# Optimization experiments

Hardware: AMD Instinct MI355X
Metric: run time of the kernel (lower is better)

Reference implementation:

```python
import jax, jax.numpy as jnp
import numpy as np
import math

B, TQ, TK, D = 4, 1024, 1024, 1024
H, DK, DV = 16, 64, 64


def _ln(x, g, b, eps=1e-5):
    m = x.mean(-1, keepdims=True)
    v = ((x - m) ** 2).mean(-1, keepdims=True)
    return (x - m) * jax.lax.rsqrt(v + eps) * g + b


def setup_inputs() -> dict:
    key = jax.random.key(0)
    ks = jax.random.split(key, 24)
    s = 0.02
    inp = {
        "x": jax.random.normal(ks[0], (B, TQ, D), jnp.float32),
        "y": jax.random.normal(ks[1], (B, TK, D), jnp.float32),
        "mask": jax.random.randint(ks[2], (B, TK), 0, 2).astype(bool),
        # pre-attention layernorms (affine)
        "ln1_g": jnp.ones((D,)), "ln1_b": jnp.zeros((D,)),
        "ln2_g": jnp.ones((D,)), "ln2_b": jnp.zeros((D,)),
        # mha1 projections
        "q_w": jax.random.normal(ks[3], (D, H * DK)) * s, "q_b": jnp.zeros((H * DK,)),
        "k_w": jax.random.normal(ks[4], (D, H * DK)) * s, "k_b": jnp.zeros((H * DK,)),
        "v_w": jax.random.normal(ks[5], (D, H * DV)) * s, "v_b": jnp.zeros((H * DV,)),
        "o_w": jax.random.normal(ks[6], (H * DV, D)) * s, "o_b": jnp.zeros((D,)),
        # MLP: [LN, ReLU, Linear] x 2 over sizes [D, D, D]
        "mln1_g": jnp.ones((D,)), "mln1_b": jnp.zeros((D,)),
        "l1_w": jax.random.normal(ks[7], (D, D)) * s, "l1_b": jnp.zeros((D,)),
        "mln2_g": jnp.ones((D,)), "mln2_b": jnp.zeros((D,)),
        "l2_w": jax.random.normal(ks[8], (D, D)) * s, "l2_b": jnp.zeros((D,)),
    }
    return inp


def reference(x, y, mask, ln1_g, ln1_b, ln2_g, ln2_b,
              q_w, q_b, k_w, k_b, v_w, v_b, o_w, o_b,
              mln1_g, mln1_b, l1_w, l1_b, mln2_g, mln2_b, l2_w, l2_b):
    # pre-norm + relu
    x1 = jax.nn.relu(_ln(x, ln1_g, ln1_b))
    y1 = jax.nn.relu(_ln(y, ln2_g, ln2_b))
    # cross attention (mha1)
    b, t, _ = x1.shape
    q = (x1 @ q_w + q_b).reshape(b, t, H, DK)
    k = (y1 @ k_w + k_b).reshape(b, -1, H, DK)
    v = (y1 @ v_w + v_b).reshape(b, -1, H, DV)
    logits = jnp.einsum('bthd,bThd->bhtT', q, k) * (1.0 / math.sqrt(DK))
    logits = jnp.where(mask[:, None, None, :], logits, -1e30)
    w = jax.nn.softmax(logits, axis=-1)
    attn = jnp.einsum('bhtT,bThd->bthd', w, v).reshape(b, t, H * DV)
    x = x + (attn @ o_w + o_b)
    # MLP: LN -> ReLU -> Linear, twice
    h = jax.nn.relu(_ln(x, mln1_g, mln1_b)) @ l1_w + l1_b
    out = jax.nn.relu(_ln(h, mln2_g, mln2_b)) @ l2_w + l2_b
    return out
```

## Files before the change

kernel.cpp:

```cpp
#include <hip/hip_runtime.h>
#include <hip/hip_bf16.h>
#include <math.h>

#define D_MODEL 1024
#define NTOK    4096

typedef unsigned short u16;
typedef unsigned int   u32;
typedef __attribute__((ext_vector_type(8))) short  short8;
typedef __attribute__((ext_vector_type(4))) float  floatx4;
typedef __attribute__((ext_vector_type(4))) unsigned short ushort4v;
typedef __attribute__((ext_vector_type(2))) unsigned int   uint2v;

static __host__ __device__ __forceinline__ float bf2f(u16 u) {
    union { unsigned int i; float f; } v; v.i = ((unsigned int)u) << 16; return v.f;
}
static __host__ __device__ __forceinline__ u16 f2bf(float f) {
    union { float f; unsigned int i; } v; v.f = f;
    unsigned int r = (v.i + 0x7FFFu + ((v.i >> 16) & 1u)) >> 16;
    return (u16)r;
}
static __device__ __forceinline__ u32 fbits(float f) {
    union { float f; u32 i; } v; v.f = f; return v.i;
}
static __device__ __forceinline__ void gl2lds16(const void* g, void* l) {
    __builtin_amdgcn_global_load_lds(
        (const __attribute__((address_space(1))) void*)g,
        (__attribute__((address_space(3))) void*)l, 16, 0, 0);
}

__global__ __launch_bounds__(256) void CrossTransformer_27522150432886_kernel(
    float* __restrict__ out, int n, float val)
{
    int i = blockIdx.x * 256 + threadIdx.x;
    if (i < n) out[i] = val;
}

__global__ __launch_bounds__(256) void mask_k(
    const void* __restrict__ mp, float* __restrict__ madd)
{
    const unsigned int* w = (const unsigned int*)mp;
    const int t = threadIdx.x;
    int bad = 0;
    for (int i = t; i < 1024; i += 256) {
        unsigned int v = w[i];
        if (!(v == 0u || v == 1u || v == 0xFFu || v == 0xFFFFFFFFu)) bad++;
    }
#pragma unroll
    for (int off = 32; off > 0; off >>= 1) bad += __shfl_xor(bad, off, 64);
    __shared__ int rb[4];
    if ((t & 63) == 0) rb[t >> 6] = bad;
    __syncthreads();
    const int Bc = rb[0] + rb[1] + rb[2] + rb[3];
    if (Bc * 2 > 1024) {
        const unsigned char* b8 = (const unsigned char*)mp;
        for (int i = t; i < 4096; i += 256) madd[i] = b8[i] ? 0.f : -1e30f;
    } else {
        const int* m32 = (const int*)mp;
        for (int i = t; i < 4096; i += 256) madd[i] = m32[i] ? 0.f : -1e30f;
    }
}

__global__ __launch_bounds__(256) void ln_relu_k(
    const void* __restrict__ in, const float* __restrict__ gam,
    const float* __restrict__ bet, u16* __restrict__ out, int bf16in)
{
    const int row = blockIdx.x, t = threadIdx.x;
    float v0, v1, v2, v3;
    if (bf16in) {
        ushort4v u = *(const ushort4v*)((const u16*)in + (size_t)row * D_MODEL + t * 4);
        v0 = bf2f(u[0]); v1 = bf2f(u[1]); v2 = bf2f(u[2]); v3 = bf2f(u[3]);
    } else {
        const float4 p = *(const float4*)((const float*)in + (size_t)row * D_MODEL + t * 4);
        v0 = p.x; v1 = p.y; v2 = p.z; v3 = p.w;
    }
    float s = v0 + v1 + v2 + v3;
    float q = v0 * v0 + v1 * v1 + v2 * v2 + v3 * v3;
#pragma unroll
    for (int off = 32; off > 0; off >>= 1) {
        s += __shfl_xor(s, off, 64);
        q += __shfl_xor(q, off, 64);
    }
    __shared__ float red[2][4];
    if ((t & 63) == 0) { red[0][t >> 6] = s; red[1][t >> 6] = q; }
    __syncthreads();
    s = red[0][0] + red[0][1] + red[0][2] + red[0][3];
    q = red[1][0] + red[1][1] + red[1][2] + red[1][3];

    const float mean = s * (1.0f / D_MODEL);
    const float var  = q * (1.0f / D_MODEL) - mean * mean;
    const float rstd = rsqrtf(var + 1e-5f);

    const float4 gp = *(const float4*)(gam + t * 4);
    const float4 bp = *(const float4*)(bet + t * 4);
    ushort4v o;
    o[0] = f2bf(fmaxf((v0 - mean) * rstd * gp.x + bp.x, 0.f));
    o[1] = f2bf(fmaxf((v1 - mean) * rstd * gp.y + bp.y, 0.f));
    o[2] = f2bf(fmaxf((v2 - mean) * rstd * gp.z + bp.z, 0.f));
    o[3] = f2bf(fmaxf((v3 - mean) * rstd * gp.w + bp.w, 0.f));
    *(ushort4v*)(out + (size_t)row * D_MODEL + t * 4) = o;
}

struct W6 { const float* w[6]; };
__global__ __launch_bounds__(256) void wtrans_k(W6 wp, u16* __restrict__ WtBase)
{
    __shared__ u16 tile[32][33];
    const float* W  = wp.w[blockIdx.z];
    u16*         Wt = WtBase + (size_t)blockIdx.z * D_MODEL * D_MODEL;
    const int c0 = blockIdx.x * 32, r0 = blockIdx.y * 32;
    const int tx = threadIdx.x, ty = threadIdx.y;
#pragma unroll
    for (int j = 0; j < 4; j++)
        tile[ty + j * 8][tx] = f2bf(W[(size_t)(r0 + ty + j * 8) * D_MODEL + c0 + tx]);
    __syncthreads();
#pragma unroll
    for (int j = 0; j < 4; j++)
        Wt[(size_t)(c0 + ty + j * 8) * D_MODEL + r0 + tx] = tile[tx][ty + j * 8];
}

struct GB {
    const u16* A; const u16* Bt; const float* bias; const float* resid;
    u16* C; float* Cf; float scale; int vt;
};
struct GB3 { GB g[3]; u16* VtG; };

__global__ __launch_bounds__(256) void gemm_qkv_k(GB3 gb)
{
    const GB cfg = gb.g[blockIdx.z];
    __shared__ __align__(16) u16 sm[3 * 8192];
    const int t = threadIdx.x, lane = t & 63, w = t >> 6;
    const int wy = w >> 1, wx = w & 1;
    const int bm = blockIdx.y * 128, bn = blockIdx.x * 128;
    const int m = lane & 15, g = lane >> 4;
    const int arow = t >> 2, aseg = (t & 3) * 8;

    const u16* Ag = cfg.A  + (size_t)(bm + arow) * D_MODEL + aseg;
    const u16* Bg = cfg.Bt + (size_t)(bn + arow) * D_MODEL + aseg;

    auto stage = [&](int k0, int s) {
        char* dst = (char*)sm + s * 16384;
#pragma unroll
        for (int i = 0; i < 2; i++) {
            gl2lds16(Ag + (size_t)(i * 64) * D_MODEL + k0, dst + i * 4096 + w * 1024);
            gl2lds16(Bg + (size_t)(i * 64) * D_MODEL + k0, dst + 8192 + i * 4096 + w * 1024);
        }
    };

    floatx4 acc[4][4] = {};
    const int NT = D_MODEL / 32;

    stage(0, 0);
    stage(32, 1);
    asm volatile("s_waitcnt vmcnt(4)" ::: "memory");
    __builtin_amdgcn_s_barrier();

    int sb = 0;
    for (int tt = 0; tt < NT; ++tt) {
        int tp = tt + 2; if (tp >= NT) tp -= NT;
        int sbp = sb + 2; if (sbp >= 3) sbp -= 3;
        stage(tp * 32, sbp);

        const u16* As = sm + sb * 8192;
        const u16* Bs = As + 4096;
        short8 af[4], bf[4];
#pragma unroll
        for (int mt = 0; mt < 4; mt++)
            af[mt] = *(const short8*)(As + (wy * 64 + mt * 16 + m) * 32 + g * 8);
#pragma unroll
        for (int nt = 0; nt < 4; nt++)
            bf[nt] = *(const short8*)(Bs + (wx * 64 + nt * 16 + m) * 32 + g * 8);

        __builtin_amdgcn_s_setprio(1);
#pragma unroll
        for (int mt = 0; mt < 4; mt++)
#pragma unroll
            for (int nt = 0; nt < 4; nt++)
                acc[mt][nt] = __builtin_amdgcn_mfma_f32_16x16x32_bf16(
                    af[mt], bf[nt], acc[mt][nt], 0, 0, 0);
        __builtin_amdgcn_s_setprio(0);

        asm volatile("s_waitcnt vmcnt(4)" ::: "memory");
        __builtin_amdgcn_s_barrier();
        sb = sb + 1; if (sb >= 3) sb -= 3;
    }
    asm volatile("s_waitcnt vmcnt(0)" ::: "memory");
    __builtin_amdgcn_s_barrier();

    float bv[4];
#pragma unroll
    for (int nt = 0; nt < 4; nt++)
        bv[nt] = cfg.bias[bn + wx * 64 + nt * 16 + m];

    if (!cfg.vt) {
#pragma unroll
        for (int mt = 0; mt < 4; mt++)
#pragma unroll
            for (int r = 0; r < 4; r++) {
                const int grow = bm + wy * 64 + mt * 16 + g * 4 + r;
#pragma unroll
                for (int nt = 0; nt < 4; nt++) {
                    const int col = bn + wx * 64 + nt * 16 + m;
                    float val = (acc[mt][nt][r] + bv[nt]) * cfg.scale;
                    cfg.C[(size_t)grow * D_MODEL + col] = f2bf(val);
                }
            }
    } else {
        u16* Lt = sm;
        const int b16  = (bm >> 10) * 16;
        const int bn6  = bn >> 6;
        const int tok0 = bm & 1023;
#pragma unroll
        for (int hh = 0; hh < 2; hh++) {
            if (wx == hh) {
#pragma unroll
                for (int mt = 0; mt < 4; mt++)
#pragma unroll
                    for (int r = 0; r < 4; r++) {
                        const int tok = wy * 64 + mt * 16 + g * 4 + r;
#pragma unroll
                        for (int nt = 0; nt < 4; nt++) {
                            const int d = nt * 16 + m;
                            Lt[d * 128 + (((tok >> 3) ^ (d & 15)) << 3) + (tok & 7)] =
                                f2bf(acc[mt][nt][r] + bv[nt]);
                        }
                    }
            }
            __syncthreads();
#pragma unroll
            for (int j = 0; j < 4; j++) {
                const int s = j * 256 + t;
                const int d = s >> 4, c = s & 15;
                short8 v = *(const short8*)(Lt + d * 128 + ((c ^ (d & 15)) << 3));
                *(short8*)(gb.VtG + ((size_t)((b16 + bn6 + hh) * 64 + d)) * 1024 + tok0 + c * 8) = v;
            }
            __syncthreads();
        }
    }
}

__global__ __launch_bounds__(256) void gemm_k(GB3 gb)
{
    const GB cfg = gb.g[blockIdx.z];
    __shared__ __align__(16) u16 sm[3 * 6144];
    const int t = threadIdx.x, lane = t & 63, w = t >> 6;
    const int wy = w >> 1, wx = w & 1;
    const int bm = blockIdx.y * 128, bn = blockIdx.x * 64;
    const int m = lane & 15, g = lane >> 4;

    const u16* Ag = cfg.A  + (size_t)(bm + (t >> 2)) * D_MODEL + (t & 3) * 8;
    const u16* Bg = cfg.Bt + (size_t)(bn + w * 16 + (lane >> 2)) * D_MODEL + (lane & 3) * 8;

    auto stage = [&](int k0, int s) {
        char* dst = (char*)sm + s * 12288;
#pragma unroll
        for (int i = 0; i < 2; i++)
            gl2lds16(Ag + (size_t)(i * 64) * D_MODEL + k0, dst + i * 4096 + w * 1024);
        gl2lds16(Bg + k0, dst + 8192 + w * 1024);
    };

    floatx4 acc[4][2] = {};
    const int NT = D_MODEL / 32;

    stage(0, 0);
    stage(32, 1);
    asm volatile("s_waitcnt vmcnt(3)" ::: "memory");
    __builtin_amdgcn_s_barrier();

    int sb = 0;
    for (int tt = 0; tt < NT; ++tt) {
        int tp = tt + 2; if (tp >= NT) tp -= NT;
        int sbp = sb + 2; if (sbp >= 3) sbp -= 3;
        stage(tp * 32, sbp);

        const u16* As = sm + sb * 6144;
        const u16* Bs = As + 4096;
        short8 af[4], bf[2];
#pragma unroll
        for (int mt = 0; mt < 4; mt++)
            af[mt] = *(const short8*)(As + (wy * 64 + mt * 16 + m) * 32 + g * 8);
#pragma unroll
        for (int nt = 0; nt < 2; nt++)
            bf[nt] = *(const short8*)(Bs + (wx * 32 + nt * 16 + m) * 32 + g * 8);

        __builtin_amdgcn_s_setprio(1);
#pragma unroll
        for (int mt = 0; mt < 4; mt++)
#pragma unroll
            for (int nt = 0; nt < 2; nt++)
                acc[mt][nt] = __builtin_amdgcn_mfma_f32_16x16x32_bf16(
                    af[mt], bf[nt], acc[mt][nt], 0, 0, 0);
        __builtin_amdgcn_s_setprio(0);

        asm volatile("s_waitcnt vmcnt(3)" ::: "memory");
        __builtin_amdgcn_s_barrier();
        sb = sb + 1; if (sb >= 3) sb -= 3;
    }
    asm volatile("s_waitcnt vmcnt(0)" ::: "memory");

    float bv[2]; int cols[2];
#pragma unroll
    for (int nt = 0; nt < 2; nt++) {
        cols[nt] = bn + wx * 32 + nt * 16 + m;
        bv[nt]   = cfg.bias[cols[nt]];
    }
#pragma unroll
    for (int mt = 0; mt < 4; mt++) {
#pragma unroll
        for (int r = 0; r < 4; r++) {
            const int grow = bm + wy * 64 + mt * 16 + g * 4 + r;
#pragma unroll
            for (int nt = 0; nt < 2; nt++) {
                float val = (acc[mt][nt][r] + bv[nt]) * cfg.scale;
                if (cfg.resid) val += cfg.resid[(size_t)grow * D_MODEL + cols[nt]];
                if (cfg.Cf) cfg.Cf[(size_t)grow * D_MODEL + cols[nt]] = val;
                else        cfg.C [(size_t)grow * D_MODEL + cols[nt]] = f2bf(val);
            }
        }
    }
}

__global__ __launch_bounds__(256) void attn_k(
    const u16* __restrict__ Q, const u16* __restrict__ Kk,
    const u16* __restrict__ VtG, const float* __restrict__ maddG,
    u16* __restrict__ Ob)
{
    __shared__ __align__(16) char smraw[41472];
    u16*   Ks   = (u16*)smraw;
    u16*   Vt   = (u16*)(smraw + 9216);
    u16*   Ps   = (u16*)(smraw + 18432);
    float* madd = (float*)(smraw + 36864);
    float* liS  = (float*)(smraw + 40960);

    const int qt = blockIdx.x, h = blockIdx.y, b = blockIdx.z;
    const int t = threadIdx.x, lane = t & 63, w = t >> 6;
    const int m = lane & 15, g = lane >> 4;

    for (int i = t; i < 1024; i += 256) madd[i] = maddG[b * 1024 + i];

    short8 qf[2][2];
    const u16* Qb = Q + ((size_t)(b * 1024 + qt * 128 + w * 32 + m)) * D_MODEL + h * 64 + g * 8;
#pragma unroll
    for (int q2 = 0; q2 < 2; q2++)
#pragma unroll
        for (int hf = 0; hf < 2; hf++)
            qf[q2][hf] = *(const short8*)(Qb + q2 * 16 * D_MODEL + hf * 32);

    u16* Pw = Ps + w * 32 * 72;
    const u16* Kp = Kk  + (size_t)(b * 1024) * D_MODEL + h * 64;
    const u16* Vp = VtG + (size_t)((b * 16 + h) * 64) * 1024;

    floatx4 Ov[2][4] = {};
    float li[2] = { 0.f, 0.f };

    for (int kt = 0; kt < 1024; kt += 64) {
#pragma unroll
        for (int i = 0; i < 2; i++) {
            const int s = i * 256 + t, row = s >> 3, seg = (s & 7) * 8;
            *(short8*)(Ks + row * 72 + seg) =
                *(const short8*)(Kp + (size_t)(kt + row) * D_MODEL + seg);
            *(short8*)(Vt + row * 72 + seg) =
                *(const short8*)(Vp + (size_t)row * 1024 + kt + seg);
        }
        __syncthreads();

        short8 af[4][2];
        float4 md[4];
#pragma unroll
        for (int tile = 0; tile < 4; tile++) {
            af[tile][0] = *(const short8*)(Ks + (tile * 16 + m) * 72 + g * 8);
            af[tile][1] = *(const short8*)(Ks + (tile * 16 + m) * 72 + 32 + g * 8);
            md[tile]    = *(const float4*)(madd + kt + tile * 16 + g * 4);
        }

#pragma unroll
        for (int q2 = 0; q2 < 2; q2++) {
            floatx4 st[4];
#pragma unroll
            for (int tile = 0; tile < 4; tile++) {
                floatx4 z = {};
                z = __builtin_amdgcn_mfma_f32_16x16x32_bf16(af[tile][0], qf[q2][0], z, 0, 0, 0);
                st[tile] = __builtin_amdgcn_mfma_f32_16x16x32_bf16(af[tile][1], qf[q2][1], z, 0, 0, 0);
            }
            float rs = 0.f;
#pragma unroll
            for (int tile = 0; tile < 4; tile++) {
                float p0 = exp2f(st[tile][0] + md[tile].x);
                float p1 = exp2f(st[tile][1] + md[tile].y);
                float p2 = exp2f(st[tile][2] + md[tile].z);
                float p3 = exp2f(st[tile][3] + md[tile].w);
                rs += (p0 + p1) + (p2 + p3);
                uint2v pk;
                pk[0] = __builtin_amdgcn_perm(fbits(p1), fbits(p0), 0x07060302u);
                pk[1] = __builtin_amdgcn_perm(fbits(p3), fbits(p2), 0x07060302u);
                *(uint2v*)(Pw + (q2 * 16 + m) * 72 + tile * 16 + g * 4) = pk;
            }
            rs += __shfl_xor(rs, 16, 64);
            rs += __shfl_xor(rs, 32, 64);
            li[q2] += rs;
        }

        short8 pa[2][2], vb[4][2];
#pragma unroll
        for (int q2 = 0; q2 < 2; q2++) {
            pa[q2][0] = *(const short8*)(Pw + (q2 * 16 + m) * 72 + g * 8);
            pa[q2][1] = *(const short8*)(Pw + (q2 * 16 + m) * 72 + 32 + g * 8);
        }
#pragma unroll
        for (int nt = 0; nt < 4; nt++) {
            vb[nt][0] = *(const short8*)(Vt + (nt * 16 + m) * 72 + g * 8);
            vb[nt][1] = *(const short8*)(Vt + (nt * 16 + m) * 72 + 32 + g * 8);
        }
#pragma unroll
        for (int q2 = 0; q2 < 2; q2++)
#pragma unroll
            for (int nt = 0; nt < 4; nt++) {
                Ov[q2][nt] = __builtin_amdgcn_mfma_f32_16x16x32_bf16(
                    pa[q2][0], vb[nt][0], Ov[q2][nt], 0, 0, 0);
                Ov[q2][nt] = __builtin_amdgcn_mfma_f32_16x16x32_bf16(
                    pa[q2][1], vb[nt][1], Ov[q2][nt], 0, 0, 0);
            }
        __syncthreads();
    }

    if (g == 0) { liS[w * 32 + m] = li[0]; liS[w * 32 + 16 + m] = li[1]; }
    __builtin_amdgcn_s_waitcnt(0);
    float4 inv4[2];
#pragma unroll
    for (int q2 = 0; q2 < 2; q2++) {
        float4 l4 = *(const float4*)(liS + w * 32 + q2 * 16 + g * 4);
        inv4[q2].x = 1.0f / fmaxf(l4.x, 1e-37f);
        inv4[q2].y = 1.0f / fmaxf(l4.y, 1e-37f);
        inv4[q2].z = 1.0f / fmaxf(l4.z, 1e-37f);
        inv4[q2].w = 1.0f / fmaxf(l4.w, 1e-37f);
    }
#pragma unroll
    for (int q2 = 0; q2 < 2; q2++) {
        const float iv[4] = { inv4[q2].x, inv4[q2].y, inv4[q2].z, inv4[q2].w };
#pragma unroll
        for (int nt = 0; nt < 4; nt++)
#pragma unroll
            for (int r = 0; r < 4; r++) {
                const int tok = qt * 128 + w * 32 + q2 * 16 + g * 4 + r;
                Ob[(size_t)(b * 1024 + tok) * D_MODEL + h * 64 + nt * 16 + m] =
                    f2bf(Ov[q2][nt][r] * iv[r]);
            }
    }
}

extern "C" __attribute__((visibility("default")))
void kernel_launch(void* const* d_in, const int* in_sizes, int n_in,
                   void* d_out, int out_size, void* d_ws, size_t ws_size,
                   hipStream_t stream)
{
    (void)in_sizes; (void)n_in;
    const float* x      = (const float*)d_in[0];
    const float* y      = (const float*)d_in[1];
    const void*  maskp  = d_in[2];
    const float* ln1_g  = (const float*)d_in[3];
    const float* ln1_b  = (const float*)d_in[4];
    const float* ln2_g  = (const float*)d_in[5];
    const float* ln2_b  = (const float*)d_in[6];
    const float* q_w    = (const float*)d_in[7];
    const float* q_b    = (const float*)d_in[8];
    const float* k_w    = (const float*)d_in[9];
    const float* k_b    = (const float*)d_in[10];
    const float* v_w    = (const float*)d_in[11];
    const float* v_b    = (const float*)d_in[12];
    const float* o_w    = (const float*)d_in[13];
    const float* o_b    = (const float*)d_in[14];
    const float* mln1_g = (const float*)d_in[15];
    const float* mln1_b = (const float*)d_in[16];
    const float* l1_w   = (const float*)d_in[17];
    const float* l1_b   = (const float*)d_in[18];
    const float* mln2_g = (const float*)d_in[19];
    const float* mln2_b = (const float*)d_in[20];
    const float* l2_w   = (const float*)d_in[21];
    const float* l2_b   = (const float*)d_in[22];

    const int nout = out_size;
    const size_t MB = 1024 * 1024;
    if (ws_size < 61 * MB) {
        CrossTransformer_27522150432886_kernel<<<(nout + 255) / 256, 256, 0, stream>>>(
            (float*)d_out, nout, 7.0f);
        return;
    }

    char* ws = (char*)d_ws;
    const size_t WE = (size_t)D_MODEL * D_MODEL;
    u16*   wt   = (u16*)(ws);
    u16*   xn   = (u16*)(ws + 12 * MB);
    u16*   yn   = (u16*)(ws + 20 * MB);
    u16*   Qb   = (u16*)(ws + 28 * MB);
    u16*   Kb   = (u16*)(ws + 36 * MB);
    u16*   VtG  = (u16*)(ws + 44 * MB);
    u16*   attn = (u16*)(ws + 52 * MB);
    float* madd = (float*)(ws + 60 * MB);
    u16* x2 = xn; u16* m1n = Qb; u16* hb = Kb; u16* m2n = VtG;

    mask_k<<<1, 256, 0, stream>>>(maskp, madd);

    W6 wp; wp.w[0] = q_w; wp.w[1] = k_w; wp.w[2] = v_w;
    wp.w[3] = o_w; wp.w[4] = l1_w; wp.w[5] = l2_w;
    wtrans_k<<<dim3(32, 32, 6), dim3(32, 8), 0, stream>>>(wp, wt);

    ln_relu_k<<<NTOK, 256, 0, stream>>>(x, ln1_g, ln1_b, xn, 0);
    ln_relu_k<<<NTOK, 256, 0, stream>>>(y, ln2_g, ln2_b, yn, 0);

    const float qscale = 0.18033688011112042f;
    GB3 qkv = {};
    qkv.g[0] = GB{ xn, wt + 0 * WE, q_b, nullptr, Qb, nullptr, qscale, 0 };
    qkv.g[1] = GB{ yn, wt + 1 * WE, k_b, nullptr, Kb, nullptr, 1.0f,  0 };
    qkv.g[2] = GB{ yn, wt + 2 * WE, v_b, nullptr, nullptr, nullptr, 1.0f, 1 };
    qkv.VtG = VtG;
    gemm_qkv_k<<<dim3(8, 32, 3), 256, 0, stream>>>(qkv);

    attn_k<<<dim3(8, 16, 4), 256, 0, stream>>>(Qb, Kb, VtG, madd, attn);

    GB3 go = {};
    go.g[0] = GB{ attn, wt + 3 * WE, o_b, x, x2, nullptr, 1.0f, 0 };
    gemm_k<<<dim3(16, 32, 1), 256, 0, stream>>>(go);

    ln_relu_k<<<NTOK, 256, 0, stream>>>(x2, mln1_g, mln1_b, m1n, 1);

    GB3 g1 = {};
    g1.g[0] = GB{ m1n, wt + 4 * WE, l1_b, nullptr, hb, nullptr, 1.0f, 0 };
    gemm_k<<<dim3(16, 32, 1), 256, 0, stream>>>(g1);

    ln_relu_k<<<NTOK, 256, 0, stream>>>(hb, mln2_g, mln2_b, m2n, 1);

    GB3 g2 = {};
    g2.g[0] = GB{ m2n, wt + 5 * WE, l2_b, nullptr, nullptr, (float*)d_out, 1.0f, 0 };
    gemm_k<<<dim3(16, 32, 1), 256, 0, stream>>>(g2);
}
```

Measured before the change: 309.4 us.

## Double-buffer attention K/V via direct-to-LDS loads and swizzle GEMM LDS layouts

The attention kernel now double-buffers K and V tiles in LDS, filling them with asynchronous global-to-LDS loads so the next tile loads while the current one computes. The padded row stride is replaced by an XOR swizzle to avoid bank conflicts. The GEMM kernels apply the same XOR swizzle to their LDS tiles, and exp2f is replaced with the raw v_exp_f32 instruction, with setprio hints around the MFMA blocks. This adds LDS usage, which may lower occupancy, and the raw exp skips exp2f's denormal and range handling.

```diff
diff --git a/kernel.cpp b/kernel.cpp
--- a/kernel.cpp
+++ b/kernel.cpp
@@ -22,6 +22,9 @@
 }
 static __device__ __forceinline__ u32 fbits(float f) {
     union { float f; u32 i; } v; v.f = f; return v.i;
+}
+static __device__ __forceinline__ float fexp2(float x) {
+    float r; asm("v_exp_f32 %0, %1" : "=v"(r) : "v"(x)); return r;
 }
 static __device__ __forceinline__ void gl2lds16(const void* g, void* l) {
     __builtin_amdgcn_global_load_lds(
@@ -132,7 +135,9 @@
     const int wy = w >> 1, wx = w & 1;
     const int bm = blockIdx.y * 128, bn = blockIdx.x * 128;
     const int m = lane & 15, g = lane >> 4;
-    const int arow = t >> 2, aseg = (t & 3) * 8;
+    const int arow = t >> 2;
+    const int aseg = ((t & 3) ^ ((t >> 3) & 3)) * 8;
+    const int gsw  = (g ^ ((m >> 1) & 3)) * 8;
 
     const u16* Ag = cfg.A  + (size_t)(bm + arow) * D_MODEL + aseg;
     const u16* Bg = cfg.Bt + (size_t)(bn + arow) * D_MODEL + aseg;
@@ -165,10 +170,10 @@
         short8 af[4], bf[4];
 #pragma unroll
         for (int mt = 0; mt < 4; mt++)
-            af[mt] = *(const short8*)(As + (wy * 64 + mt * 16 + m) * 32 + g * 8);
+            af[mt] = *(const short8*)(As + (wy * 64 + mt * 16 + m) * 32 + gsw);
 #pragma unroll
         for (int nt = 0; nt < 4; nt++)
-            bf[nt] = *(const short8*)(Bs + (wx * 64 + nt * 16 + m) * 32 + g * 8);
+            bf[nt] = *(const short8*)(Bs + (wx * 64 + nt * 16 + m) * 32 + gsw);
 
         __builtin_amdgcn_s_setprio(1);
 #pragma unroll
@@ -246,9 +251,12 @@
     const int wy = w >> 1, wx = w & 1;
     const int bm = blockIdx.y * 128, bn = blockIdx.x * 64;
     const int m = lane & 15, g = lane >> 4;
-
-    const u16* Ag = cfg.A  + (size_t)(bm + (t >> 2)) * D_MODEL + (t & 3) * 8;
-    const u16* Bg = cfg.Bt + (size_t)(bn + w * 16 + (lane >> 2)) * D_MODEL + (lane & 3) * 8;
+    const int gsw = (g ^ ((m >> 1) & 3)) * 8;
+
+    const u16* Ag = cfg.A  + (size_t)(bm + (t >> 2)) * D_MODEL
+                    + ((t & 3) ^ ((t >> 3) & 3)) * 8;
+    const u16* Bg = cfg.Bt + (size_t)(bn + w * 16 + (lane >> 2)) * D_MODEL
+                    + ((lane & 3) ^ ((lane >> 3) & 3)) * 8;
 
     auto stage = [&](int k0, int s) {
         char* dst = (char*)sm + s * 12288;
@@ -277,10 +285,10 @@
         short8 af[4], bf[2];
 #pragma unroll
         for (int mt = 0; mt < 4; mt++)
-            af[mt] = *(const short8*)(As + (wy * 64 + mt * 16 + m) * 32 + g * 8);
+            af[mt] = *(const short8*)(As + (wy * 64 + mt * 16 + m) * 32 + gsw);
 #pragma unroll
         for (int nt = 0; nt < 2; nt++)
-            bf[nt] = *(const short8*)(Bs + (wx * 32 + nt * 16 + m) * 32 + g * 8);
+            bf[nt] = *(const short8*)(Bs + (wx * 32 + nt * 16 + m) * 32 + gsw);
 
         __builtin_amdgcn_s_setprio(1);
 #pragma unroll
@@ -324,12 +332,12 @@
     const u16* __restrict__ VtG, const float* __restrict__ maddG,
     u16* __restrict__ Ob)
 {
-    __shared__ __align__(16) char smraw[41472];
-    u16*   Ks   = (u16*)smraw;
-    u16*   Vt   = (u16*)(smraw + 9216);
-    u16*   Ps   = (u16*)(smraw + 18432);
-    float* madd = (float*)(smraw + 36864);
-    float* liS  = (float*)(smraw + 40960);
+    __shared__ __align__(16) char smraw[55808];
+    u16*   KsB  = (u16*)smraw;
+    u16*   VtB  = (u16*)(smraw + 16384);
+    u16*   Ps   = (u16*)(smraw + 32768);
+    float* madd = (float*)(smraw + 51200);
+    float* liS  = (float*)(smraw + 55296);
 
     const int qt = blockIdx.x, h = blockIdx.y, b = blockIdx.z;
     const int t = threadIdx.x, lane = t & 63, w = t >> 6;
@@ -349,45 +357,63 @@
     const u16* Kp = Kk  + (size_t)(b * 1024) * D_MODEL + h * 64;
     const u16* Vp = VtG + (size_t)((b * 16 + h) * 64) * 1024;
 
+    const int r0 = lane >> 3;
+    const int ssl = ((lane & 7) ^ r0) * 8;
+    auto stageKV = [&](int kt, int bufI) {
+#pragma unroll
+        for (int i = 0; i < 2; i++) {
+            const int row = w * 16 + i * 8 + r0;
+            gl2lds16(Kp + (size_t)(kt + row) * D_MODEL + ssl,
+                     (char*)(KsB + bufI * 4096) + (w * 2 + i) * 1024);
+            gl2lds16(Vp + (size_t)row * 1024 + kt + ssl,
+                     (char*)(VtB + bufI * 4096) + (w * 2 + i) * 1024);
+        }
+    };
+
     floatx4 Ov[2][4] = {};
     float li[2] = { 0.f, 0.f };
 
+    const int s8  = m & 7;
+    const int sl0 = (g ^ s8) * 8;
+    const int sl1 = sl0 ^ 32;
+
+    stageKV(0, 0);
+    __syncthreads();
+
+    int buf = 0;
     for (int kt = 0; kt < 1024; kt += 64) {
-#pragma unroll
-        for (int i = 0; i < 2; i++) {
-            const int s = i * 256 + t, row = s >> 3, seg = (s & 7) * 8;
-            *(short8*)(Ks + row * 72 + seg) =
-                *(const short8*)(Kp + (size_t)(kt + row) * D_MODEL + seg);
-            *(short8*)(Vt + row * 72 + seg) =
-                *(const short8*)(Vp + (size_t)row * 1024 + kt + seg);
-        }
-        __syncthreads();
+        if (kt + 64 < 1024) stageKV(kt + 64, buf ^ 1);
+
+        const u16* Ks = KsB + buf * 4096;
+        const u16* Vt = VtB + buf * 4096;
 
         short8 af[4][2];
         float4 md[4];
 #pragma unroll
         for (int tile = 0; tile < 4; tile++) {
-            af[tile][0] = *(const short8*)(Ks + (tile * 16 + m) * 72 + g * 8);
-            af[tile][1] = *(const short8*)(Ks + (tile * 16 + m) * 72 + 32 + g * 8);
+            af[tile][0] = *(const short8*)(Ks + (tile * 16 + m) * 64 + sl0);
+            af[tile][1] = *(const short8*)(Ks + (tile * 16 + m) * 64 + sl1);
             md[tile]    = *(const float4*)(madd + kt + tile * 16 + g * 4);
         }
 
 #pragma unroll
         for (int q2 = 0; q2 < 2; q2++) {
             floatx4 st[4];
+            __builtin_amdgcn_s_setprio(1);
 #pragma unroll
             for (int tile = 0; tile < 4; tile++) {
                 floatx4 z = {};
                 z = __builtin_amdgcn_mfma_f32_16x16x32_bf16(af[tile][0], qf[q2][0], z, 0, 0, 0);
                 st[tile] = __builtin_amdgcn_mfma_f32_16x16x32_bf16(af[tile][1], qf[q2][1], z, 0, 0, 0);
             }
+            __builtin_amdgcn_s_setprio(0);
             float rs = 0.f;
 #pragma unroll
             for (int tile = 0; tile < 4; tile++) {
-                float p0 = exp2f(st[tile][0] + md[tile].x);
-                float p1 = exp2f(st[tile][1] + md[tile].y);
-                float p2 = exp2f(st[tile][2] + md[tile].z);
-                float p3 = exp2f(st[tile][3] + md[tile].w);
+                float p0 = fexp2(st[tile][0] + md[tile].x);
+                float p1 = fexp2(st[tile][1] + md[tile].y);
+                float p2 = fexp2(st[tile][2] + md[tile].z);
+                float p3 = fexp2(st[tile][3] + md[tile].w);
                 rs += (p0 + p1) + (p2 + p3);
                 uint2v pk;
                 pk[0] = __builtin_amdgcn_perm(fbits(p1), fbits(p0), 0x07060302u);
@@ -407,9 +433,10 @@
         }
 #pragma unroll
         for (int nt = 0; nt < 4; nt++) {
-            vb[nt][0] = *(const short8*)(Vt + (nt * 16 + m) * 72 + g * 8);
-            vb[nt][1] = *(const short8*)(Vt + (nt * 16 + m) * 72 + 32 + g * 8);
-        }
+            vb[nt][0] = *(const short8*)(Vt + (nt * 16 + m) * 64 + sl0);
+            vb[nt][1] = *(const short8*)(Vt + (nt * 16 + m) * 64 + sl1);
+        }
+        __builtin_amdgcn_s_setprio(1);
 #pragma unroll
         for (int q2 = 0; q2 < 2; q2++)
 #pragma unroll
@@ -419,7 +446,11 @@
                 Ov[q2][nt] = __builtin_amdgcn_mfma_f32_16x16x32_bf16(
                     pa[q2][1], vb[nt][1], Ov[q2][nt], 0, 0, 0);
             }
-        __syncthreads();
+        __builtin_amdgcn_s_setprio(0);
+
+        asm volatile("s_waitcnt vmcnt(0)" ::: "memory");
+        __builtin_amdgcn_s_barrier();
+        buf ^= 1;
     }
 
     if (g == 0) { liS[w * 32 + m] = li[0]; liS[w * 32 + 16 + m] = li[1]; }
```

After: 305.0 us. No clear change (-1.4%).
